# Performance work log

Measured on AMD Instinct MI355X. Metric: run time of the kernel, lower is better.

Reference implementation:

```python
import jax, jax.numpy as jnp
import numpy as np

B, N, F_IN, H = 1, 8192, 128, 64
NEG_INF = -1e9


def setup_inputs() -> dict:
    key = jax.random.key(0)
    ks = jax.random.split(key, 6)
    seq = jax.random.normal(ks[0], (B, N, F_IN), dtype=jnp.float32)
    # sparse-ish binary adjacency (~avg degree 64) with self loops
    adj = (jax.random.uniform(ks[1], (B, N, N)) < (64.0 / N)).astype(jnp.float32)
    eye = jnp.eye(N, dtype=jnp.float32)[None]
    adj = jnp.maximum(adj, eye)
    bias_mat = NEG_INF * (1.0 - adj)  # standard GAT bias mask
    W = jax.random.normal(ks[2], (F_IN, H), dtype=jnp.float32) * 0.08
    a1_w = jax.random.normal(ks[3], (H, 1), dtype=jnp.float32) * 0.1
    a2_w = jax.random.normal(ks[4], (H, 1), dtype=jnp.float32) * 0.1
    a1_b = jnp.zeros((1,), dtype=jnp.float32)
    a2_b = jnp.zeros((1,), dtype=jnp.float32)
    bias_zero = jnp.zeros((H,), dtype=jnp.float32)
    return {"seq": seq, "adj": adj, "bias_mat": bias_mat, "W": W,
            "a1_w": a1_w, "a1_b": a1_b, "a2_w": a2_w, "a2_b": a2_b,
            "bias_zero": bias_zero}


def reference(seq, adj, bias_mat, W, a1_w, a1_b, a2_w, a2_b, bias_zero):
    # Conv1D(kernel=1) == per-node linear projection
    seq_fts = jnp.einsum('bnf,fh->bnh', seq, W)          # [B,N,H]
    f1 = jnp.einsum('bnh,ho->bno', seq_fts, a1_w) + a1_b  # [B,N,1]
    f2 = jnp.einsum('bnh,ho->bno', seq_fts, a2_w) + a2_b  # [B,N,1]
    logits = f1 + jnp.swapaxes(f2, 1, 2)                  # [B,N,N] additive GAT logits
    # NOTE: module multiplies leaky_relu(logits) by dense adj, then adds bias_mat
    scores = jax.nn.leaky_relu(logits, 0.2) * adj + bias_mat
    coefs = jax.nn.softmax(scores, axis=-1)               # [B,N,N]
    vals = jnp.einsum('bnm,bmh->bnh', coefs, seq_fts)     # weighted aggregation
    ret = vals + bias_zero
    return jax.nn.elu(ret)
```

## Files before the change

kernel.cpp:

```cpp
#include <hip/hip_runtime.h>
#include <math.h>

#define NN 8192
#define FIN 128
#define HH 64
#define CAP 128
#define PROJ_BLOCKS 512
#define SCAN_BLOCKS 2048

typedef float f32x4 __attribute__((ext_vector_type(4)));

__global__ __launch_bounds__(256, 6) void proj_scan_kernel(
    const float* __restrict__ seq, const float* __restrict__ adj,
    const float* __restrict__ W,
    const float* __restrict__ a1_w, const float* __restrict__ a1_b,
    const float* __restrict__ a2_w, const float* __restrict__ a2_b,
    float* __restrict__ seq_fts, float* __restrict__ f1, float* __restrict__ f2,
    int* __restrict__ cnt_g, unsigned short* __restrict__ jb_g)
{
    const int wave = threadIdx.x >> 6;
    const int lane = threadIdx.x & 63;
    const int b    = blockIdx.x;

    if ((b % 5) == 4) {
        const int base = (b / 5) * 16 + wave * 4;
        const float* __restrict__ s0 = seq + (size_t)(base + 0) * FIN;
        const float* __restrict__ s1 = seq + (size_t)(base + 1) * FIN;
        const float* __restrict__ s2 = seq + (size_t)(base + 2) * FIN;
        const float* __restrict__ s3 = seq + (size_t)(base + 3) * FIN;

        float a0 = 0.f, a1 = 0.f, a2 = 0.f, a3 = 0.f;
        #pragma unroll
        for (int f = 0; f < FIN; ++f) {
            const float wf = W[f * HH + lane];
            a0 = fmaf(s0[f], wf, a0);
            a1 = fmaf(s1[f], wf, a1);
            a2 = fmaf(s2[f], wf, a2);
            a3 = fmaf(s3[f], wf, a3);
        }
        seq_fts[(size_t)(base + 0) * HH + lane] = a0;
        seq_fts[(size_t)(base + 1) * HH + lane] = a1;
        seq_fts[(size_t)(base + 2) * HH + lane] = a2;
        seq_fts[(size_t)(base + 3) * HH + lane] = a3;

        const float w1 = a1_w[lane], w2 = a2_w[lane];
        float p10 = a0 * w1, p11 = a1 * w1, p12 = a2 * w1, p13 = a3 * w1;
        float p20 = a0 * w2, p21 = a1 * w2, p22 = a2 * w2, p23 = a3 * w2;
        #pragma unroll
        for (int off = 32; off >= 1; off >>= 1) {
            p10 += __shfl_xor(p10, off, 64);  p11 += __shfl_xor(p11, off, 64);
            p12 += __shfl_xor(p12, off, 64);  p13 += __shfl_xor(p13, off, 64);
            p20 += __shfl_xor(p20, off, 64);  p21 += __shfl_xor(p21, off, 64);
            p22 += __shfl_xor(p22, off, 64);  p23 += __shfl_xor(p23, off, 64);
        }
        if (lane == 0) {
            const float b1 = a1_b[0], b2 = a2_b[0];
            f1[base + 0] = p10 + b1;  f1[base + 1] = p11 + b1;
            f1[base + 2] = p12 + b1;  f1[base + 3] = p13 + b1;
            f2[base + 0] = p20 + b2;  f2[base + 1] = p21 + b2;
            f2[base + 2] = p22 + b2;  f2[base + 3] = p23 + b2;
        }
        return;
    }

    const int row = (b - b / 5) * 4 + wave;
    const f32x4* __restrict__ arow = (const f32x4*)(adj + (size_t)row * NN);

    unsigned mask0 = 0, mask1 = 0, mask2 = 0, mask3 = 0;
    #pragma unroll
    for (int c = 0; c < 32; ++c) {
        const f32x4 a = __builtin_nontemporal_load(arow + c * 64 + lane);
        const unsigned bits = (unsigned)a.x | ((unsigned)a.y << 1)
                            | ((unsigned)a.z << 2) | ((unsigned)a.w << 3);
        const unsigned sh = (unsigned)((c & 7) * 4);
        if      (c <  8) mask0 |= bits << sh;
        else if (c < 16) mask1 |= bits << sh;
        else if (c < 24) mask2 |= bits << sh;
        else             mask3 |= bits << sh;
    }

    const int cnt = __popc(mask0) + __popc(mask1) + __popc(mask2) + __popc(mask3);
    int incl = cnt;
    #pragma unroll
    for (int off = 1; off < 64; off <<= 1) {
        const int u = __shfl_up(incl, off, 64);
        if (lane >= off) incl += u;
    }
    if (lane == 63) cnt_g[row] = incl;
    int p = incl - cnt;

    unsigned short* __restrict__ jrow = jb_g + (size_t)row * CAP;
    #define DECODE(MW, W_) do {                                              \
        unsigned m_ = (MW);                                                  \
        while (m_) {                                                         \
            const int b_ = __builtin_ctz(m_);  m_ &= m_ - 1;                 \
            const int j_ = ((((W_) * 8 + (b_ >> 2)) * 64 + lane) << 2) + (b_ & 3); \
            if (p < CAP) jrow[p] = (unsigned short)j_;                       \
            ++p;                                                             \
        }                                                                    \
    } while (0)
    DECODE(mask0, 0); DECODE(mask1, 1); DECODE(mask2, 2); DECODE(mask3, 3);
    #undef DECODE
}

__global__ __launch_bounds__(256, 6) void gather_kernel(
    const float* __restrict__ seq_fts, const float* __restrict__ f1,
    const float* __restrict__ f2, const int* __restrict__ cnt_g,
    const unsigned short* __restrict__ jb_g,
    const float* __restrict__ bias_zero, float* __restrict__ out)
{
    const int wave = threadIdx.x >> 6;
    const int lane = threadIdx.x & 63;
    const int row  = blockIdx.x * 4 + wave;

    __shared__ int   jbuf[4][CAP];
    __shared__ float sbuf[4][CAP];

    const int n = min(cnt_g[row], CAP);
    const float f1i = f1[row];
    const unsigned short* __restrict__ jrow = jb_g + (size_t)row * CAP;

    float m = -1e30f;
    for (int q = lane; q < n; q += 64) {
        const int j = jrow[q];
        jbuf[wave][q] = j;
        const float x = f1i + f2[j];
        const float s = (x >= 0.f) ? x : 0.2f * x;
        sbuf[wave][q] = s;
        m = fmaxf(m, s);
    }
    #pragma unroll
    for (int off = 32; off >= 1; off >>= 1) m = fmaxf(m, __shfl_xor(m, off, 64));

    float d = 0.f;
    for (int q = lane; q < n; q += 64) {
        const float e = __expf(sbuf[wave][q] - m);
        sbuf[wave][q] = e;
        d += e;
    }
    #pragma unroll
    for (int off = 32; off >= 1; off >>= 1) d += __shfl_xor(d, off, 64);

    float acc0 = 0.f, acc1 = 0.f, acc2 = 0.f, acc3 = 0.f;
    float acc4 = 0.f, acc5 = 0.f, acc6 = 0.f, acc7 = 0.f;
    int q = 0;
    for (; q + 7 < n; q += 8) {
        acc0 = fmaf(sbuf[wave][q+0], seq_fts[(size_t)jbuf[wave][q+0] * HH + lane], acc0);
        acc1 = fmaf(sbuf[wave][q+1], seq_fts[(size_t)jbuf[wave][q+1] * HH + lane], acc1);
        acc2 = fmaf(sbuf[wave][q+2], seq_fts[(size_t)jbuf[wave][q+2] * HH + lane], acc2);
        acc3 = fmaf(sbuf[wave][q+3], seq_fts[(size_t)jbuf[wave][q+3] * HH + lane], acc3);
        acc4 = fmaf(sbuf[wave][q+4], seq_fts[(size_t)jbuf[wave][q+4] * HH + lane], acc4);
        acc5 = fmaf(sbuf[wave][q+5], seq_fts[(size_t)jbuf[wave][q+5] * HH + lane], acc5);
        acc6 = fmaf(sbuf[wave][q+6], seq_fts[(size_t)jbuf[wave][q+6] * HH + lane], acc6);
        acc7 = fmaf(sbuf[wave][q+7], seq_fts[(size_t)jbuf[wave][q+7] * HH + lane], acc7);
    }
    for (; q < n; ++q)
        acc0 = fmaf(sbuf[wave][q], seq_fts[(size_t)jbuf[wave][q] * HH + lane], acc0);

    const float v = (((acc0 + acc1) + (acc2 + acc3)) + ((acc4 + acc5) + (acc6 + acc7))) / d
                    + bias_zero[lane];
    out[(size_t)row * HH + lane] = (v > 0.f) ? v : expm1f(v);
}

extern "C" void kernel_launch(void* const* d_in, const int* in_sizes, int n_in,
                              void* d_out, int out_size, void* d_ws, size_t ws_size,
                              hipStream_t stream) {
    const float* seq       = (const float*)d_in[0];
    const float* adj       = (const float*)d_in[1];
    const float* W         = (const float*)d_in[3];
    const float* a1_w      = (const float*)d_in[4];
    const float* a1_b      = (const float*)d_in[5];
    const float* a2_w      = (const float*)d_in[6];
    const float* a2_b      = (const float*)d_in[7];
    const float* bias_zero = (const float*)d_in[8];
    float* out = (float*)d_out;

    char* ws = (char*)d_ws;
    float* seq_fts        = (float*)ws;
    float* f1             = (float*)(ws + 2097152);
    float* f2             = (float*)(ws + 2097152 + 32768);
    int*   cnt_g          = (int*)  (ws + 2097152 + 65536);
    unsigned short* jb_g  = (unsigned short*)(ws + 2097152 + 98304);

    proj_scan_kernel<<<PROJ_BLOCKS + SCAN_BLOCKS, 256, 0, stream>>>(
        seq, adj, W, a1_w, a1_b, a2_w, a2_b, seq_fts, f1, f2, cnt_g, jb_g);
    gather_kernel<<<NN / 4, 256, 0, stream>>>(
        seq_fts, f1, f2, cnt_g, jb_g, bias_zero, out);
}
```

Baseline: 70.49 us.

## Stage adjacency scan through LDS with async global_load_lds double buffering

Replaces the direct nontemporal vector loads of each adjacency row with asynchronous global-to-LDS loads (global_load_lds, 16 bytes per lane) into a per-wave double buffer. Chunks are processed while the next chunk is in flight, with manual vmcnt waits and sched barriers. The goal is deeper memory-level parallelism and lower register pressure on the bandwidth-bound adjacency scan. In exchange it uses 64 KB of LDS per block and drops the occupancy hint, which may reduce resident blocks, and the LDS reads are done without an explicit barrier, relying on per-wave ordering.

New measurement: 61.44 us (median of 2 runs). -12.8%, faster.

```diff
diff --git a/kernel.cpp b/kernel.cpp
--- a/kernel.cpp
+++ b/kernel.cpp
@@ -9,8 +9,10 @@
 #define SCAN_BLOCKS 2048
 
 typedef float f32x4 __attribute__((ext_vector_type(4)));
-
-__global__ __launch_bounds__(256, 6) void proj_scan_kernel(
+typedef const __attribute__((address_space(1))) unsigned int gu32;
+typedef __attribute__((address_space(3))) unsigned int lu32;
+
+__global__ __launch_bounds__(256) void proj_scan_kernel(
     const float* __restrict__ seq, const float* __restrict__ adj,
     const float* __restrict__ W,
     const float* __restrict__ a1_w, const float* __restrict__ a1_b,
@@ -18,6 +20,8 @@
     float* __restrict__ seq_fts, float* __restrict__ f1, float* __restrict__ f2,
     int* __restrict__ cnt_g, unsigned short* __restrict__ jb_g)
 {
+    __shared__ f32x4 stage[4][2][512];
+
     const int wave = threadIdx.x >> 6;
     const int lane = threadIdx.x & 63;
     const int b    = blockIdx.x;
@@ -64,20 +68,50 @@
     }
 
     const int row = (b - b / 5) * 4 + wave;
-    const f32x4* __restrict__ arow = (const f32x4*)(adj + (size_t)row * NN);
-
-    unsigned mask0 = 0, mask1 = 0, mask2 = 0, mask3 = 0;
-    #pragma unroll
-    for (int c = 0; c < 32; ++c) {
-        const f32x4 a = __builtin_nontemporal_load(arow + c * 64 + lane);
-        const unsigned bits = (unsigned)a.x | ((unsigned)a.y << 1)
-                            | ((unsigned)a.z << 2) | ((unsigned)a.w << 3);
-        const unsigned sh = (unsigned)((c & 7) * 4);
-        if      (c <  8) mask0 |= bits << sh;
-        else if (c < 16) mask1 |= bits << sh;
-        else if (c < 24) mask2 |= bits << sh;
-        else             mask3 |= bits << sh;
-    }
+    const char* __restrict__ g = (const char*)(adj + (size_t)row * NN);
+
+    #define ISSUE(C_) do {                                                       \
+        const char* src_ = g + (C_) * 8192 + lane * 16;                          \
+        f32x4* dst_ = &stage[wave][(C_) & 1][0];                                 \
+        _Pragma("unroll")                                                        \
+        for (int i_ = 0; i_ < 8; ++i_) {                                         \
+            __builtin_amdgcn_global_load_lds((gu32*)(src_ + i_ * 1024),          \
+                                             (lu32*)((char*)dst_ + i_ * 1024),   \
+                                             16, 0, 0);                          \
+        }                                                                        \
+    } while (0)
+
+    #define PROCESS(C_, MW_) do {                                                \
+        unsigned mw_ = 0;                                                        \
+        _Pragma("unroll")                                                        \
+        for (int i_ = 0; i_ < 8; ++i_) {                                         \
+            const f32x4 a_ = stage[wave][(C_) & 1][i_ * 64 + lane];              \
+            const unsigned bits_ = (unsigned)a_.x | ((unsigned)a_.y << 1)        \
+                                 | ((unsigned)a_.z << 2) | ((unsigned)a_.w << 3);\
+            mw_ |= bits_ << (i_ * 4);                                            \
+        }                                                                        \
+        (MW_) = mw_;                                                             \
+    } while (0)
+
+    #define WAITV(N_) do {                                                       \
+        asm volatile("s_waitcnt vmcnt(" #N_ ")" ::: "memory");                   \
+        __builtin_amdgcn_sched_barrier(0);                                       \
+    } while (0)
+
+    unsigned mask0, mask1, mask2, mask3;
+    ISSUE(0); ISSUE(1);
+    WAITV(8);
+    PROCESS(0, mask0);
+    __builtin_amdgcn_sched_barrier(0);
+    ISSUE(2);
+    WAITV(8);
+    PROCESS(1, mask1);
+    __builtin_amdgcn_sched_barrier(0);
+    ISSUE(3);
+    WAITV(8);
+    PROCESS(2, mask2);
+    WAITV(0);
+    PROCESS(3, mask3);
 
     const int cnt = __popc(mask0) + __popc(mask1) + __popc(mask2) + __popc(mask3);
     int incl = cnt;
@@ -101,6 +135,9 @@
     } while (0)
     DECODE(mask0, 0); DECODE(mask1, 1); DECODE(mask2, 2); DECODE(mask3, 3);
     #undef DECODE
+    #undef ISSUE
+    #undef PROCESS
+    #undef WAITV
 }
 
 __global__ __launch_bounds__(256, 6) void gather_kernel(
```
